# Kernel tuning notes

Hardware: AMD Instinct MI355X
Metric: run time of the kernel (lower is better)

## Reference

```python
import jax, jax.numpy as jnp
import numpy as np

VOCAB_SIZE = 50000
B, T, L, OOV = 16, 64, 400, 100  # batch, max_dec_len, max_enc_len, batch_oov_len


def setup_inputs() -> dict:
    key = jax.random.key(0)
    k0, k1, k2, k3 = jax.random.split(key, 4)
    vocab_dists = jax.random.uniform(k0, (B, T, VOCAB_SIZE), dtype=jnp.float32)
    attn_dists = jax.random.uniform(k1, (B, T, L), dtype=jnp.float32)
    p_gens = jax.random.uniform(k2, (B, T, 1), dtype=jnp.float32)
    enc_extended_inp = jax.random.randint(k3, (B, L), 0, VOCAB_SIZE + OOV, dtype=jnp.int64)
    return {
        "vocab_dists": vocab_dists,
        "attn_dists": attn_dists,
        "p_gens": p_gens,
        "enc_extended_inp": enc_extended_inp,
        "batch_oov_len": OOV,
    }


def reference(vocab_dists, attn_dists, p_gens, enc_extended_inp, batch_oov_len):
    # vocab_dists: [B, T, V]; attn_dists: [B, T, L]; p_gens: [B, T, 1]
    # enc_extended_inp: [B, L] int ids in [0, V + batch_oov_len)
    Bv, Tv, V = vocab_dists.shape
    Vext = V + batch_oov_len

    vocab = p_gens * vocab_dists                 # weighted generation dist
    attn = (1.0 - p_gens) * attn_dists           # weighted copy dist

    # extend vocab dist with zeros for in-article OOV slots
    vocab_ext = jnp.pad(vocab, ((0, 0), (0, 0), (0, batch_oov_len)))  # [B, T, Vext]

    # scatter-add copy probabilities into extended vocab (duplicates accumulate,
    # matching tf.scatter_nd semantics)
    def scatter_one(ids, a):  # ids: [L], a: [T, L] -> [T, Vext]
        return jnp.zeros((a.shape[0], Vext), a.dtype).at[:, ids].add(a)

    proj = jax.vmap(scatter_one)(enc_extended_inp, attn)  # [B, T, Vext]

    return vocab_ext + proj
```

## Files before the change

kernel.cpp:

```cpp
#include <hip/hip_runtime.h>


typedef float float4v __attribute__((ext_vector_type(4)));

__global__ __launch_bounds__(256) void pgn_fused_kernel(
    const float* __restrict__ vocab,
    const float* __restrict__ attn,
    const float* __restrict__ pg,
    const int* __restrict__ ids,
    float* __restrict__ out,
    int T, int L, int V4, int Vext4) {
  const int row = blockIdx.x;
  const float p = pg[row];

  const float4v* __restrict__ vrow =
      reinterpret_cast<const float4v*>(vocab) + (long)row * V4;
  float4v* __restrict__ orow4 =
      reinterpret_cast<float4v*>(out) + (long)row * Vext4;

  for (int c = threadIdx.x; c < Vext4; c += 256) {
    float4v o;
    if (c < V4) {
      const float4v v = __builtin_nontemporal_load(vrow + c);
      o = v * p;
    } else {
      o = (float4v)(0.f);
    }
    orow4[c] = o;
  }

  __syncthreads();

  const float q = 1.0f - p;
  const int b = row / T;
  float* __restrict__ orow = out + (long)row * (Vext4 * 4);
  const float* __restrict__ arow = attn + (long)row * L;
  const int* __restrict__ irow = ids + (long)b * L;

  for (int l = threadIdx.x; l < L; l += 256) {
    atomicAdd(orow + irow[l], q * arow[l]);
  }
}

extern "C" void kernel_launch(void* const* d_in, const int* in_sizes, int n_in,
                              void* d_out, int out_size, void* d_ws, size_t ws_size,
                              hipStream_t stream) {
  const float* vocab = (const float*)d_in[0];
  const float* attn  = (const float*)d_in[1];
  const float* pg    = (const float*)d_in[2];
  const int*   ids   = (const int*)d_in[3];
  float* out = (float*)d_out;

  const int BT   = in_sizes[2];
  const int V    = in_sizes[0] / BT;
  const int L    = in_sizes[1] / BT;
  const int Vext = out_size / BT;
  const int B    = in_sizes[3] / L;
  const int T    = BT / B;

  const int V4 = V / 4, Vext4 = Vext / 4;

  pgn_fused_kernel<<<BT, 256, 0, stream>>>(vocab, attn, pg, ids, out,
                                           T, L, V4, Vext4);
}
```

Before: 81.31 us.

## Accumulate copy scatter in LDS chunks and fuse with vocab scaling store

Each row's extended vocab is processed in LDS chunks of about 40KB. The chunk is zeroed, the scatter-add of copy probabilities is done with LDS atomics, and then the result plus the scaled vocab is written once with nontemporal stores. This removes the second pass of global atomics and the read-after-write to global memory, but adds several block barriers per chunk and a large LDS footprint that may lower occupancy. The code assumes L is at most 512.

After: 88.20 us. +8.5%, slower.

```diff
diff --git a/kernel.cpp b/kernel.cpp
--- a/kernel.cpp
+++ b/kernel.cpp
@@ -3,42 +3,63 @@
 
 typedef float float4v __attribute__((ext_vector_type(4)));
 
-__global__ __launch_bounds__(256) void pgn_fused_kernel(
+constexpr int TPB    = 256;
+constexpr int CHUNK4 = 2505;
+constexpr int ITERS  = (CHUNK4 + TPB - 1) / TPB;
+
+__global__ __launch_bounds__(TPB) void pgn_fused_lds_kernel(
     const float* __restrict__ vocab,
     const float* __restrict__ attn,
     const float* __restrict__ pg,
     const int* __restrict__ ids,
     float* __restrict__ out,
     int T, int L, int V4, int Vext4) {
+  __shared__ float4v lds[CHUNK4];
+
   const int row = blockIdx.x;
+  const int tid = threadIdx.x;
   const float p = pg[row];
+  const float q = 1.0f - p;
+  const int b = row / T;
+
+  const float* __restrict__ arow = attn + (long)row * L;
+  const int* __restrict__ irow = ids + (long)b * L;
+  int id0 = -1, id1 = -1;
+  float s0 = 0.f, s1 = 0.f;
+  if (tid < L)       { id0 = irow[tid];       s0 = q * arow[tid]; }
+  if (tid + TPB < L) { id1 = irow[tid + TPB]; s1 = q * arow[tid + TPB]; }
 
   const float4v* __restrict__ vrow =
       reinterpret_cast<const float4v*>(vocab) + (long)row * V4;
-  float4v* __restrict__ orow4 =
+  float4v* __restrict__ orow =
       reinterpret_cast<float4v*>(out) + (long)row * Vext4;
+  float* ldsf = reinterpret_cast<float*>(lds);
 
-  for (int c = threadIdx.x; c < Vext4; c += 256) {
-    float4v o;
-    if (c < V4) {
-      const float4v v = __builtin_nontemporal_load(vrow + c);
-      o = v * p;
-    } else {
-      o = (float4v)(0.f);
+  for (int lo4 = 0; lo4 < Vext4; lo4 += CHUNK4) {
+    const int hi4 = min(lo4 + CHUNK4, Vext4);
+    const int lof = lo4 * 4, hif = hi4 * 4;
+
+    #pragma unroll
+    for (int i = 0; i < ITERS; ++i) {
+      const int c = tid + i * TPB;
+      if (c < CHUNK4) lds[c] = (float4v)(0.f);
     }
-    orow4[c] = o;
-  }
+    __syncthreads();
 
-  __syncthreads();
+    if (id0 >= lof && id0 < hif) atomicAdd(ldsf + (id0 - lof), s0);
+    if (id1 >= lof && id1 < hif) atomicAdd(ldsf + (id1 - lof), s1);
+    __syncthreads();
 
-  const float q = 1.0f - p;
-  const int b = row / T;
-  float* __restrict__ orow = out + (long)row * (Vext4 * 4);
-  const float* __restrict__ arow = attn + (long)row * L;
-  const int* __restrict__ irow = ids + (long)b * L;
-
-  for (int l = threadIdx.x; l < L; l += 256) {
-    atomicAdd(orow + irow[l], q * arow[l]);
+    #pragma unroll
+    for (int i = 0; i < ITERS; ++i) {
+      const int c4 = lo4 + tid + i * TPB;
+      if (c4 < hi4) {
+        float4v o = lds[c4 - lo4];
+        if (c4 < V4) o += p * __builtin_nontemporal_load(vrow + c4);
+        __builtin_nontemporal_store(o, orow + c4);
+      }
+    }
+    __syncthreads();
   }
 }
 
@@ -60,6 +81,6 @@
 
   const int V4 = V / 4, Vext4 = Vext / 4;
 
-  pgn_fused_kernel<<<BT, 256, 0, stream>>>(vocab, attn, pg, ids, out,
-                                           T, L, V4, Vext4);
+  pgn_fused_lds_kernel<<<BT, TPB, 0, stream>>>(vocab, attn, pg, ids, out,
+                                               T, L, V4, Vext4);
 }
```

## Split rows into chunks and accumulate scatter in LDS before single write

Applied to the files above, without the earlier changes.

Each row is now split across five blocks, one per vocabulary chunk. Each block zeroes an LDS buffer for its chunk, scatter-adds the copy probabilities that land in that chunk using LDS atomics, then streams the chunk once, adding the scaled vocab and writing the output. This removes the separate global atomic pass, which had to re-touch output memory after the main write, and gives the grid five times more blocks. In exchange, every block rereads all L ids, and about 40KB of LDS per block may limit occupancy. CHUNK4 and NCHUNK are hardcoded for this vocabulary size.

Result: faster. 77.17 us (-5.1%).

```diff
diff --git a/kernel.cpp b/kernel.cpp
--- a/kernel.cpp
+++ b/kernel.cpp
@@ -3,42 +3,52 @@
 
 typedef float float4v __attribute__((ext_vector_type(4)));
 
-__global__ __launch_bounds__(256) void pgn_fused_kernel(
+constexpr int TPB    = 256;
+constexpr int CHUNK4 = 2505;
+constexpr int CHUNKF = CHUNK4 * 4;
+constexpr int NCHUNK = 5;
+
+__global__ __launch_bounds__(TPB) void pgn_chunk_lds_kernel(
     const float* __restrict__ vocab,
     const float* __restrict__ attn,
     const float* __restrict__ pg,
     const int* __restrict__ ids,
     float* __restrict__ out,
     int T, int L, int V4, int Vext4) {
-  const int row = blockIdx.x;
+  __shared__ float lds[CHUNKF];
+  float4v* lds4 = reinterpret_cast<float4v*>(lds);
+
+  const int chunk = blockIdx.x;
+  const int row   = blockIdx.y;
+  const int tid   = threadIdx.x;
+
+  const int lo4 = chunk * CHUNK4;
+  const int hi4 = min(lo4 + CHUNK4, Vext4);
+  const int lof = lo4 * 4, hif = hi4 * 4;
+
   const float p = pg[row];
+  const float q = 1.0f - p;
+  const int b = row / T;
+
+  for (int c = tid; c < CHUNK4; c += TPB) lds4[c] = (float4v)(0.f);
+  __syncthreads();
+
+  const float* __restrict__ arow = attn + (long)row * L;
+  const int* __restrict__ irow = ids + (long)b * L;
+  for (int l = tid; l < L; l += TPB) {
+    const int id = irow[l];
+    if (id >= lof && id < hif) atomicAdd(lds + (id - lof), q * arow[l]);
+  }
+  __syncthreads();
 
   const float4v* __restrict__ vrow =
       reinterpret_cast<const float4v*>(vocab) + (long)row * V4;
-  float4v* __restrict__ orow4 =
+  float4v* __restrict__ orow =
       reinterpret_cast<float4v*>(out) + (long)row * Vext4;
-
-  for (int c = threadIdx.x; c < Vext4; c += 256) {
-    float4v o;
-    if (c < V4) {
-      const float4v v = __builtin_nontemporal_load(vrow + c);
-      o = v * p;
-    } else {
-      o = (float4v)(0.f);
-    }
-    orow4[c] = o;
-  }
-
-  __syncthreads();
-
-  const float q = 1.0f - p;
-  const int b = row / T;
-  float* __restrict__ orow = out + (long)row * (Vext4 * 4);
-  const float* __restrict__ arow = attn + (long)row * L;
-  const int* __restrict__ irow = ids + (long)b * L;
-
-  for (int l = threadIdx.x; l < L; l += 256) {
-    atomicAdd(orow + irow[l], q * arow[l]);
+  for (int c4 = lo4 + tid; c4 < hi4; c4 += TPB) {
+    float4v o = lds4[c4 - lo4];
+    if (c4 < V4) o += p * __builtin_nontemporal_load(vrow + c4);
+    orow[c4] = o;
   }
 }
 
@@ -60,6 +70,7 @@
 
   const int V4 = V / 4, Vext4 = Vext / 4;
 
-  pgn_fused_kernel<<<BT, 256, 0, stream>>>(vocab, attn, pg, ids, out,
-                                           T, L, V4, Vext4);
+  dim3 grid(NCHUNK, BT);
+  pgn_chunk_lds_kernel<<<grid, TPB, 0, stream>>>(vocab, attn, pg, ids, out,
+                                                 T, L, V4, Vext4);
 }
```
